# Kernel optimization log

Measured on AMD Instinct MI355X. Metric: run time of the kernel, lower is better.

The kernel has to match this reference:

```python
import jax, jax.numpy as jnp
import numpy as np

IN_F = 4096
OUT_F = 11008
GROUP = 128
NG = IN_F // GROUP  # 32 groups


def setup_inputs() -> dict:
    key = jax.random.key(0)
    k1, k2, k3, k4 = jax.random.split(key, 4)
    x = jax.random.normal(k1, (4, 2048, IN_F), dtype=jnp.float32)
    # packed 4-bit weights: 8 nibbles per int32 along the in_features axis
    qweight = jax.random.randint(k2, (IN_F // 8, OUT_F), 0, 2**31 - 1, dtype=jnp.int32)
    scales = jax.random.uniform(k3, (NG, OUT_F), dtype=jnp.float32, minval=0.001, maxval=0.02)
    # packed 4-bit zero-points: 8 nibbles per int32 along the out_features axis
    qzeros = jax.random.randint(k4, (NG, OUT_F // 8), 0, 2**31 - 1, dtype=jnp.int32)
    g_idx = (jnp.arange(IN_F) // GROUP).astype(jnp.int32)
    return {"x": x, "qweight": qweight, "scales": scales, "qzeros": qzeros, "g_idx": g_idx}


def _dequant(qweight, scales, qzeros, g_idx):
    """GPTQ v2 dequant (matches vecquant4recons_v2): W = s * (w4 - (z4 + 1))."""
    shifts = (jnp.arange(8, dtype=jnp.uint32) * 4)  # nibble shifts 0..28
    qw = jax.lax.bitcast_convert_type(qweight, jnp.uint32)  # [in/8, out]
    # unpack along in_features: [in/8, 8, out] -> [in, out]
    w4 = ((qw[:, None, :] >> shifts[None, :, None]) & jnp.uint32(0xF)).reshape(-1, qweight.shape[1])
    qz = jax.lax.bitcast_convert_type(qzeros, jnp.uint32)  # [ng, out/8]
    # unpack along out_features: [ng, out/8, 8] -> [ng, out]; GPTQ adds +1 to zero
    z4 = ((qz[:, :, None] >> shifts[None, None, :]) & jnp.uint32(0xF)).reshape(qzeros.shape[0], -1) + jnp.uint32(1)
    dt = scales.dtype
    return scales[g_idx] * (w4.astype(dt) - z4[g_idx].astype(dt))  # [in, out]


def reference(x, qweight, scales, qzeros, g_idx):
    W = _dequant(qweight, scales, qzeros, g_idx)  # [in_features, out_features]
    return jnp.matmul(x, W)  # [..., out_features]
```

## Files before the change

### kernel.cpp

```cpp
#include <hip/hip_runtime.h>
#include <hip/hip_fp16.h>
#include <stdint.h>


#define IN_F  4096
#define OUT_F 11008

typedef __attribute__((ext_vector_type(8))) _Float16 half8;
typedef __attribute__((ext_vector_type(4))) float f32x4;

__device__ __forceinline__ __half2 u2h2(uint32_t u) {
    union { uint32_t u; __half2 h; } c; c.u = u; return c.h;
}
__device__ __forceinline__ uint32_t h22u(__half2 h) {
    union { uint32_t u; __half2 h; } c; c.h = h; return c.u;
}
__device__ __forceinline__ uint32_t pkrtz(float lo, float hi) {
    union { __fp16 h[2]; uint32_t u; } c;
    *(decltype(__builtin_amdgcn_cvt_pkrtz(0.f,0.f))*)c.h =
        __builtin_amdgcn_cvt_pkrtz(lo, hi);
    return c.u;
}
__device__ __forceinline__ void async_copy16(const void* gsrc, void* ldst) {
    __builtin_amdgcn_global_load_lds(
        (const __attribute__((address_space(1))) uint32_t*)gsrc,
        (__attribute__((address_space(3))) uint32_t*)ldst,
        16, 0, 0);
}

__global__ __launch_bounds__(256) void cvt_a(
    const float* __restrict__ x, uint4* __restrict__ xh)
{
    const size_t idx = (size_t)blockIdx.x * 256 + threadIdx.x;
    const float4* p = (const float4*)(x + idx * 8);
    const float4 lo = p[0], hi = p[1];
    uint4 w;
    w.x = pkrtz(lo.x, hi.x);
    w.y = pkrtz(lo.y, hi.y);
    w.z = pkrtz(lo.z, hi.z);
    w.w = pkrtz(lo.w, hi.w);
    xh[idx] = w;
}

__global__ __launch_bounds__(512, 2) void gptq_gemm256(
    const uint4* __restrict__ xh,
    const int*   __restrict__ qweight,
    const float* __restrict__ scales,
    const int*   __restrict__ qzeros,
    float* __restrict__ out)
{
    extern __shared__ uint4 smem[];

    const int t    = threadIdx.x;
    const int lane = t & 63;
    const int wave = t >> 6;
    const int n0   = blockIdx.x * 256;
    const int m0   = blockIdx.y * 256;

    const int wm   = (wave >> 2) * 128;
    const int wn   = (wave & 3) * 64;
    const int ln15 = lane & 15;
    const int quad = lane >> 4;
    const int swz  = ln15 & 7;

    f32x4 acc[8][4];
#pragma unroll
    for (int i = 0; i < 8; ++i)
#pragma unroll
        for (int j = 0; j < 4; ++j)
            acc[i][j] = (f32x4){0.f, 0.f, 0.f, 0.f};

    const int arow_l = lane >> 3;
    const int xch    = (lane & 7) ^ arow_l;
    const char* asrc[4];
#pragma unroll
    for (int q = 0; q < 4; ++q) {
        const int m = wave * 32 + q * 8 + arow_l;
        asrc[q] = (const char*)xh + ((size_t)(m0 + m) * 512 + xch) * 16;
    }
    const int aslot = (wave * 4) * 64;

    const int b_c  = t & 255;
    const int b_r0 = t >> 8;
    const int n_th = n0 + b_c;
    const int*   qw_base = qweight + n_th;
    const float* sc_base = scales + n_th;
    const int*   qz_base = qzeros + (n_th >> 3);
    const int    z_shift = (n_th & 7) * 4;

    {
        uint32_t bw[4];
#pragma unroll
        for (int i = 0; i < 4; ++i)
            bw[i] = (uint32_t)qw_base[(size_t)(b_r0 + 2 * i) * OUT_F];
        const float    s  = sc_base[0];
        const uint32_t zw = (uint32_t)qz_base[0];
#pragma unroll
        for (int q = 0; q < 4; ++q) {
            async_copy16(asrc[q], smem + aslot + q * 64);
            asrc[q] += 128;
        }
        const __half2 s2  = u2h2(pkrtz(s, s));
        const float   bzf = (float)(((zw >> z_shift) & 0xFu) + 1025u);
        const __half2 bz2 = u2h2(pkrtz(bzf, bzf));
        uint4* Bb = smem + 4096;
#pragma unroll
        for (int i = 0; i < 4; ++i) {
            const int r = b_r0 + 2 * i;
            const uint32_t w = bw[i];
            uint32_t q0 = ( w        & 0x000F000Fu) | 0x64006400u;
            uint32_t q1 = ((w >>  4) & 0x000F000Fu) | 0x64006400u;
            uint32_t q2 = ((w >>  8) & 0x000F000Fu) | 0x64006400u;
            uint32_t q3 = ((w >> 12) & 0x000F000Fu) | 0x64006400u;
            uint4 o;
            o.x = h22u(__hmul2(__hsub2(u2h2(q0), bz2), s2));
            o.y = h22u(__hmul2(__hsub2(u2h2(q1), bz2), s2));
            o.z = h22u(__hmul2(__hsub2(u2h2(q2), bz2), s2));
            o.w = h22u(__hmul2(__hsub2(u2h2(q3), bz2), s2));
            Bb[b_c * 8 + (r ^ (b_c & 7))] = o;
        }
        __syncthreads();
    }

    for (int tile = 0; tile < 64; ++tile) {
        const int  cur = tile & 1;
        const int  nxt = cur ^ 1;
        const bool pf  = (tile < 63);

        uint32_t nbw[4]; float ns = 0.f; uint32_t nzw = 0;
        if (pf) {
            const int kq0 = (tile + 1) * 8;
#pragma unroll
            for (int i = 0; i < 4; ++i)
                nbw[i] = (uint32_t)qw_base[(size_t)(kq0 + b_r0 + 2 * i) * OUT_F];
            const int g = (tile + 1) >> 1;
            ns  = sc_base[(size_t)g * OUT_F];
            nzw = (uint32_t)qz_base[(size_t)g * (OUT_F / 8)];
            uint4* An = smem + (nxt ? 2048 : 0);
#pragma unroll
            for (int q = 0; q < 4; ++q) {
                async_copy16(asrc[q], An + aslot + q * 64);
                asrc[q] += 128;
            }
        }

        const uint4* Ac = smem + (cur ? 2048 : 0);
        const uint4* Bc = smem + 4096 + (cur ? 2048 : 0);
#pragma unroll
        for (int ks = 0; ks < 2; ++ks) {
            half8 af[8], bf[4];
#pragma unroll
            for (int i = 0; i < 8; ++i) {
                const int m  = wm + i * 16 + ln15;
                const int ch = (ks * 4 + quad) ^ swz;
                af[i] = *(const half8*)&Ac[m * 8 + ch];
            }
#pragma unroll
            for (int j = 0; j < 4; ++j) {
                const int n  = wn + j * 16 + ln15;
                const int ch = (ks * 4 + quad) ^ swz;
                bf[j] = *(const half8*)&Bc[n * 8 + ch];
            }
#pragma unroll
            for (int i = 0; i < 8; ++i)
#pragma unroll
                for (int j = 0; j < 4; ++j)
                    acc[i][j] = __builtin_amdgcn_mfma_f32_16x16x32_f16(
                        af[i], bf[j], acc[i][j], 0, 0, 0);
        }

        if (pf) {
            const __half2 s2  = u2h2(pkrtz(ns, ns));
            const float   bzf = (float)(((nzw >> z_shift) & 0xFu) + 1025u);
            const __half2 bz2 = u2h2(pkrtz(bzf, bzf));
            uint4* Bn = smem + 4096 + (nxt ? 2048 : 0);
#pragma unroll
            for (int i = 0; i < 4; ++i) {
                const int r = b_r0 + 2 * i;
                const uint32_t w = nbw[i];
                uint32_t q0 = ( w        & 0x000F000Fu) | 0x64006400u;
                uint32_t q1 = ((w >>  4) & 0x000F000Fu) | 0x64006400u;
                uint32_t q2 = ((w >>  8) & 0x000F000Fu) | 0x64006400u;
                uint32_t q3 = ((w >> 12) & 0x000F000Fu) | 0x64006400u;
                uint4 o;
                o.x = h22u(__hmul2(__hsub2(u2h2(q0), bz2), s2));
                o.y = h22u(__hmul2(__hsub2(u2h2(q1), bz2), s2));
                o.z = h22u(__hmul2(__hsub2(u2h2(q2), bz2), s2));
                o.w = h22u(__hmul2(__hsub2(u2h2(q3), bz2), s2));
                Bn[b_c * 8 + (r ^ (b_c & 7))] = o;
            }
            __syncthreads();
        }
    }

#pragma unroll
    for (int i = 0; i < 8; ++i) {
#pragma unroll
        for (int j = 0; j < 4; ++j) {
            const int col  = n0 + wn + j * 16 + ln15;
            const int row0 = m0 + wm + i * 16 + quad * 4;
            float* p = out + (size_t)row0 * OUT_F + col;
#pragma unroll
            for (int r = 0; r < 4; ++r)
                p[(size_t)r * OUT_F] = acc[i][j][r];
        }
    }
}

__global__ __launch_bounds__(256, 4) void gptq_gemm(
    const float* __restrict__ x,
    const int*   __restrict__ qweight,
    const float* __restrict__ scales,
    const int*   __restrict__ qzeros,
    float* __restrict__ out)
{
    __shared__ uint4 As[128 * 8];
    __shared__ uint4 Bs[128 * 8];

    const int t    = threadIdx.x;
    const int lane = t & 63;
    const int wave = t >> 6;
    const int n0   = blockIdx.x * 128;
    const int m0   = blockIdx.y * 128;

    const int wm   = (wave >> 1) * 64;
    const int wn   = (wave & 1) * 64;
    const int ln15 = lane & 15;
    const int quad = lane >> 4;

    f32x4 acc[4][4];
#pragma unroll
    for (int i = 0; i < 4; ++i)
#pragma unroll
        for (int j = 0; j < 4; ++j)
            acc[i][j] = (f32x4){0.f, 0.f, 0.f, 0.f};

    const int a_m0 = t >> 3;
    const int a_c8 = t & 7;
    const float* x_base = x + (size_t)(m0 + a_m0) * IN_F + a_c8 * 8;

    const int b_c  = t & 127;
    const int b_r0 = t >> 7;
    const int n_th = n0 + b_c;
    const int*   qw_base = qweight + n_th;
    const float* sc_base = scales + n_th;
    const int*   qz_base = qzeros + (n_th >> 3);
    const int    z_shift = (n_th & 7) * 4;

    for (int k0 = 0; k0 < IN_F; k0 += 64) {
        float4 av[8];
#pragma unroll
        for (int i = 0; i < 4; ++i) {
            const float* p = x_base + (size_t)(32 * i) * IN_F + k0;
            av[2 * i]     = *(const float4*)p;
            av[2 * i + 1] = *(const float4*)(p + 4);
        }
        const int kq0 = k0 >> 3;
        uint32_t bw[4];
#pragma unroll
        for (int i = 0; i < 4; ++i)
            bw[i] = (uint32_t)qw_base[(size_t)(kq0 + b_r0 + 2 * i) * OUT_F];

        const int g = k0 >> 7;
        const float    s  = sc_base[(size_t)g * OUT_F];
        const uint32_t zw = (uint32_t)qz_base[(size_t)g * (OUT_F / 8)];
        const float    bzf = (float)(((zw >> z_shift) & 0xFu) + 1025u);
        const __half2  s2  = u2h2(pkrtz(s, s));
        const __half2  bz2 = u2h2(pkrtz(bzf, bzf));

        __syncthreads();

#pragma unroll
        for (int i = 0; i < 4; ++i) {
            const int m  = a_m0 + 32 * i;
            const int ch = a_c8 ^ (m & 7);
            const float4 lo = av[2 * i], hi = av[2 * i + 1];
            uint4 w;
            w.x = pkrtz(lo.x, hi.x);
            w.y = pkrtz(lo.y, hi.y);
            w.z = pkrtz(lo.z, hi.z);
            w.w = pkrtz(lo.w, hi.w);
            As[m * 8 + ch] = w;
        }
#pragma unroll
        for (int i = 0; i < 4; ++i) {
            const int r = b_r0 + 2 * i;
            const uint32_t w = bw[i];
            uint32_t q0 = ( w        & 0x000F000Fu) | 0x64006400u;
            uint32_t q1 = ((w >>  4) & 0x000F000Fu) | 0x64006400u;
            uint32_t q2 = ((w >>  8) & 0x000F000Fu) | 0x64006400u;
            uint32_t q3 = ((w >> 12) & 0x000F000Fu) | 0x64006400u;
            uint4 o;
            o.x = h22u(__hmul2(__hsub2(u2h2(q0), bz2), s2));
            o.y = h22u(__hmul2(__hsub2(u2h2(q1), bz2), s2));
            o.z = h22u(__hmul2(__hsub2(u2h2(q2), bz2), s2));
            o.w = h22u(__hmul2(__hsub2(u2h2(q3), bz2), s2));
            const int ch = r ^ (b_c & 7);
            Bs[b_c * 8 + ch] = o;
        }
        __syncthreads();

#pragma unroll
        for (int ks = 0; ks < 2; ++ks) {
            half8 af[4], bf[4];
#pragma unroll
            for (int i = 0; i < 4; ++i) {
                const int m  = wm + i * 16 + ln15;
                const int ch = (ks * 4 + quad) ^ (m & 7);
                af[i] = *(const half8*)&As[m * 8 + ch];
            }
#pragma unroll
            for (int j = 0; j < 4; ++j) {
                const int n  = wn + j * 16 + ln15;
                const int ch = (ks * 4 + quad) ^ (n & 7);
                bf[j] = *(const half8*)&Bs[n * 8 + ch];
            }
#pragma unroll
            for (int i = 0; i < 4; ++i)
#pragma unroll
                for (int j = 0; j < 4; ++j)
                    acc[i][j] = __builtin_amdgcn_mfma_f32_16x16x32_f16(
                        af[i], bf[j], acc[i][j], 0, 0, 0);
        }
    }

#pragma unroll
    for (int i = 0; i < 4; ++i) {
#pragma unroll
        for (int j = 0; j < 4; ++j) {
            const int col  = n0 + wn + j * 16 + ln15;
            const int row0 = m0 + wm + i * 16 + quad * 4;
            float* p = out + (size_t)row0 * OUT_F + col;
#pragma unroll
            for (int r = 0; r < 4; ++r)
                p[(size_t)r * OUT_F] = acc[i][j][r];
        }
    }
}

extern "C" void kernel_launch(void* const* d_in, const int* in_sizes, int n_in,
                              void* d_out, int out_size, void* d_ws, size_t ws_size,
                              hipStream_t stream) {
    const float* x       = (const float*)d_in[0];
    const int*   qweight = (const int*)d_in[1];
    const float* scales  = (const float*)d_in[2];
    const int*   qzeros  = (const int*)d_in[3];
    float* out = (float*)d_out;

    const size_t xh_bytes = (size_t)8192 * IN_F * 2;
    if (d_ws != nullptr && ws_size >= xh_bytes) {
        static bool attr_done = false;
        if (!attr_done) {
            (void)hipFuncSetAttribute(
                reinterpret_cast<const void*>(gptq_gemm256),
                hipFuncAttributeMaxDynamicSharedMemorySize, 131072);
            attr_done = true;
        }
        uint4* xh = (uint4*)d_ws;
        cvt_a<<<(8192 * 512) / 256, 256, 0, stream>>>(x, xh);
        dim3 grid(OUT_F / 256, 8192 / 256);
        gptq_gemm256<<<grid, 512, 131072, stream>>>(xh, qweight, scales, qzeros, out);
    } else {
        dim3 grid(OUT_F / 128, 8192 / 128);
        gptq_gemm<<<grid, 256, 0, stream>>>(x, qweight, scales, qzeros, out);
    }
}
```

Baseline: 1.148 ms.

## Split tile loop into four phased MFMA blocks with barriers and priority

Restructures each K-tile into four phases, each of which reads a quarter of the A/B fragments from LDS, issues part of the async A prefetch or the B dequant, then runs 16 MFMAs under raised s_setprio between explicit barriers and waitcnts. The goal is to interleave LDS reads, global prefetch and dequant work with MFMA execution across waves, as in ping-pong scheduling. It adds several workgroup barriers per tile, which could stall waves if the phases are not balanced.

```diff
diff --git a/kernel.cpp b/kernel.cpp
--- a/kernel.cpp
+++ b/kernel.cpp
@@ -42,6 +42,32 @@
     xh[idx] = w;
 }
 
+
+#define READ_A4(DST, AC, I0, KS)                                         \
+    _Pragma("unroll") for (int i_ = 0; i_ < 4; ++i_) {                   \
+        const int m_ = wm + ((I0) + i_) * 16 + ln15;                     \
+        DST[i_] = *(const half8*)&AC[m_ * 8 + (((KS) * 4 + quad) ^ swz)];\
+    }
+#define READ_B4(DST, BC, KS)                                             \
+    _Pragma("unroll") for (int j_ = 0; j_ < 4; ++j_) {                   \
+        const int n_ = wn + j_ * 16 + ln15;                              \
+        DST[j_] = *(const half8*)&BC[n_ * 8 + (((KS) * 4 + quad) ^ swz)];\
+    }
+#define MFMA16(I0, AV, BV)                                               \
+    _Pragma("unroll") for (int i_ = 0; i_ < 4; ++i_)                     \
+    _Pragma("unroll") for (int j_ = 0; j_ < 4; ++j_)                     \
+        acc[(I0) + i_][j_] = __builtin_amdgcn_mfma_f32_16x16x32_f16(     \
+            AV[i_], BV[j_], acc[(I0) + i_][j_], 0, 0, 0);
+#define PHASE_MFMA(I0, AV, BV)                                           \
+    __builtin_amdgcn_sched_barrier(0);                                   \
+    __builtin_amdgcn_s_barrier();                                        \
+    asm volatile("s_waitcnt lgkmcnt(0)" ::: "memory");                   \
+    __builtin_amdgcn_sched_barrier(0);                                   \
+    __builtin_amdgcn_s_setprio(1);                                       \
+    MFMA16(I0, AV, BV);                                                  \
+    __builtin_amdgcn_s_setprio(0);                                       \
+    __builtin_amdgcn_sched_barrier(0);
+
 __global__ __launch_bounds__(512, 2) void gptq_gemm256(
     const uint4* __restrict__ xh,
     const int*   __restrict__ qweight,
@@ -78,7 +104,7 @@
         const int m = wave * 32 + q * 8 + arow_l;
         asrc[q] = (const char*)xh + ((size_t)(m0 + m) * 512 + xch) * 16;
     }
-    const int aslot = (wave * 4) * 64;
+    const int aslot = wave * 256;
 
     const int b_c  = t & 255;
     const int b_r0 = t >> 8;
@@ -126,8 +152,16 @@
         const int  cur = tile & 1;
         const int  nxt = cur ^ 1;
         const bool pf  = (tile < 63);
+        const uint4* Ac = smem + (cur ? 2048 : 0);
+        const uint4* Bc = smem + 4096 + (cur ? 2048 : 0);
+        uint4* An = smem + (nxt ? 2048 : 0);
+        uint4* Bn = smem + 4096 + (nxt ? 2048 : 0);
 
         uint32_t nbw[4]; float ns = 0.f; uint32_t nzw = 0;
+
+        half8 a0[4], b0[4];
+        READ_A4(a0, Ac, 0, 0);
+        READ_B4(b0, Bc, 0);
         if (pf) {
             const int kq0 = (tile + 1) * 8;
 #pragma unroll
@@ -136,44 +170,33 @@
             const int g = (tile + 1) >> 1;
             ns  = sc_base[(size_t)g * OUT_F];
             nzw = (uint32_t)qz_base[(size_t)g * (OUT_F / 8)];
-            uint4* An = smem + (nxt ? 2048 : 0);
-#pragma unroll
-            for (int q = 0; q < 4; ++q) {
-                async_copy16(asrc[q], An + aslot + q * 64);
-                asrc[q] += 128;
-            }
-        }
-
-        const uint4* Ac = smem + (cur ? 2048 : 0);
-        const uint4* Bc = smem + 4096 + (cur ? 2048 : 0);
-#pragma unroll
-        for (int ks = 0; ks < 2; ++ks) {
-            half8 af[8], bf[4];
-#pragma unroll
-            for (int i = 0; i < 8; ++i) {
-                const int m  = wm + i * 16 + ln15;
-                const int ch = (ks * 4 + quad) ^ swz;
-                af[i] = *(const half8*)&Ac[m * 8 + ch];
-            }
-#pragma unroll
-            for (int j = 0; j < 4; ++j) {
-                const int n  = wn + j * 16 + ln15;
-                const int ch = (ks * 4 + quad) ^ swz;
-                bf[j] = *(const half8*)&Bc[n * 8 + ch];
-            }
-#pragma unroll
-            for (int i = 0; i < 8; ++i)
-#pragma unroll
-                for (int j = 0; j < 4; ++j)
-                    acc[i][j] = __builtin_amdgcn_mfma_f32_16x16x32_f16(
-                        af[i], bf[j], acc[i][j], 0, 0, 0);
-        }
-
+            async_copy16(asrc[0], An + aslot);       asrc[0] += 128;
+            async_copy16(asrc[1], An + aslot + 64);  asrc[1] += 128;
+        }
+        PHASE_MFMA(0, a0, b0);
+        __builtin_amdgcn_s_barrier();
+
+        half8 a1[4];
+        READ_A4(a1, Ac, 4, 0);
+        if (pf) {
+            async_copy16(asrc[2], An + aslot + 128); asrc[2] += 128;
+            async_copy16(asrc[3], An + aslot + 192); asrc[3] += 128;
+        }
+        PHASE_MFMA(4, a1, b0);
+        __builtin_amdgcn_s_barrier();
+
+        half8 a2[4], b1[4];
+        READ_A4(a2, Ac, 0, 1);
+        READ_B4(b1, Bc, 1);
+        PHASE_MFMA(0, a2, b1);
+        __builtin_amdgcn_s_barrier();
+
+        half8 a3[4];
+        READ_A4(a3, Ac, 4, 1);
         if (pf) {
             const __half2 s2  = u2h2(pkrtz(ns, ns));
             const float   bzf = (float)(((nzw >> z_shift) & 0xFu) + 1025u);
             const __half2 bz2 = u2h2(pkrtz(bzf, bzf));
-            uint4* Bn = smem + 4096 + (nxt ? 2048 : 0);
 #pragma unroll
             for (int i = 0; i < 4; ++i) {
                 const int r = b_r0 + 2 * i;
@@ -189,8 +212,9 @@
                 o.w = h22u(__hmul2(__hsub2(u2h2(q3), bz2), s2));
                 Bn[b_c * 8 + (r ^ (b_c & 7))] = o;
             }
-            __syncthreads();
-        }
+        }
+        PHASE_MFMA(4, a3, b1);
+        __syncthreads();
     }
 
 #pragma unroll
```

Measured after the change: 1.164 ms. Within noise of the previous version (+1.3%).

## Dequantize weights directly into MFMA B-fragments in registers, drop B LDS staging

Applied to the files above, without the earlier changes.

The 256-tile kernel no longer stages dequantized weights through shared memory. Each lane now loads the packed int4 words it needs for its MFMA B operands straight from global memory and dequantizes them in registers, keeping scale and zero per column and reloading them only at group boundaries. Dynamic LDS drops from 128 KB to 64 KB, which removes the B LDS writes and reads and could allow more resident blocks. In exchange, each weight word is loaded and dequantized redundantly by every wave that shares the column, global loads become narrower and less coalesced, and register pressure rises.

```diff
diff --git a/kernel.cpp b/kernel.cpp
--- a/kernel.cpp
+++ b/kernel.cpp
@@ -5,6 +5,7 @@
 
 #define IN_F  4096
 #define OUT_F 11008
+#define QZ_W  (OUT_F / 8)
 
 typedef __attribute__((ext_vector_type(8))) _Float16 half8;
 typedef __attribute__((ext_vector_type(4))) float f32x4;
@@ -26,6 +27,18 @@
         (const __attribute__((address_space(1))) uint32_t*)gsrc,
         (__attribute__((address_space(3))) uint32_t*)ldst,
         16, 0, 0);
+}
+__device__ __forceinline__ half8 dq8(uint32_t w, __half2 bz2, __half2 s2) {
+    uint32_t q0 = ( w        & 0x000F000Fu) | 0x64006400u;
+    uint32_t q1 = ((w >>  4) & 0x000F000Fu) | 0x64006400u;
+    uint32_t q2 = ((w >>  8) & 0x000F000Fu) | 0x64006400u;
+    uint32_t q3 = ((w >> 12) & 0x000F000Fu) | 0x64006400u;
+    union { half8 h; uint32_t u[4]; } f;
+    f.u[0] = h22u(__hmul2(__hsub2(u2h2(q0), bz2), s2));
+    f.u[1] = h22u(__hmul2(__hsub2(u2h2(q1), bz2), s2));
+    f.u[2] = h22u(__hmul2(__hsub2(u2h2(q2), bz2), s2));
+    f.u[3] = h22u(__hmul2(__hsub2(u2h2(q3), bz2), s2));
+    return f.h;
 }
 
 __global__ __launch_bounds__(256) void cvt_a(
@@ -78,119 +91,112 @@
         const int m = wave * 32 + q * 8 + arow_l;
         asrc[q] = (const char*)xh + ((size_t)(m0 + m) * 512 + xch) * 16;
     }
-    const int aslot = (wave * 4) * 64;
-
-    const int b_c  = t & 255;
-    const int b_r0 = t >> 8;
-    const int n_th = n0 + b_c;
-    const int*   qw_base = qweight + n_th;
-    const float* sc_base = scales + n_th;
-    const int*   qz_base = qzeros + (n_th >> 3);
-    const int    z_shift = (n_th & 7) * 4;
-
-    {
-        uint32_t bw[4];
-#pragma unroll
-        for (int i = 0; i < 4; ++i)
-            bw[i] = (uint32_t)qw_base[(size_t)(b_r0 + 2 * i) * OUT_F];
-        const float    s  = sc_base[0];
-        const uint32_t zw = (uint32_t)qz_base[0];
-#pragma unroll
-        for (int q = 0; q < 4; ++q) {
-            async_copy16(asrc[q], smem + aslot + q * 64);
-            asrc[q] += 128;
-        }
-        const __half2 s2  = u2h2(pkrtz(s, s));
-        const float   bzf = (float)(((zw >> z_shift) & 0xFu) + 1025u);
-        const __half2 bz2 = u2h2(pkrtz(bzf, bzf));
-        uint4* Bb = smem + 4096;
-#pragma unroll
-        for (int i = 0; i < 4; ++i) {
-            const int r = b_r0 + 2 * i;
-            const uint32_t w = bw[i];
-            uint32_t q0 = ( w        & 0x000F000Fu) | 0x64006400u;
-            uint32_t q1 = ((w >>  4) & 0x000F000Fu) | 0x64006400u;
-            uint32_t q2 = ((w >>  8) & 0x000F000Fu) | 0x64006400u;
-            uint32_t q3 = ((w >> 12) & 0x000F000Fu) | 0x64006400u;
-            uint4 o;
-            o.x = h22u(__hmul2(__hsub2(u2h2(q0), bz2), s2));
-            o.y = h22u(__hmul2(__hsub2(u2h2(q1), bz2), s2));
-            o.z = h22u(__hmul2(__hsub2(u2h2(q2), bz2), s2));
-            o.w = h22u(__hmul2(__hsub2(u2h2(q3), bz2), s2));
-            Bb[b_c * 8 + (r ^ (b_c & 7))] = o;
-        }
-        __syncthreads();
-    }
+    const int aslot = wave * 256;
+
+    const int* qwp[4];
+    int sc_ix[4], qz_ix[4], zsh[4];
+#pragma unroll
+    for (int j = 0; j < 4; ++j) {
+        const int nj = n0 + wn + j * 16 + ln15;
+        qwp[j]   = qweight + (size_t)quad * OUT_F + nj;
+        sc_ix[j] = nj;
+        qz_ix[j] = nj >> 3;
+        zsh[j]   = (nj & 7) * 4;
+    }
+
+    uint32_t bw[2][4];
+#pragma unroll
+    for (int ks = 0; ks < 2; ++ks)
+#pragma unroll
+        for (int j = 0; j < 4; ++j)
+            bw[ks][j] = (uint32_t)qwp[j][(size_t)(ks * 4) * OUT_F];
+
+    __half2 s2[4], bz2[4];
+#pragma unroll
+    for (int j = 0; j < 4; ++j) {
+        const float    s  = scales[sc_ix[j]];
+        const uint32_t zw = (uint32_t)qzeros[qz_ix[j]];
+        s2[j]  = u2h2(pkrtz(s, s));
+        const float bzf = (float)(((zw >> zsh[j]) & 0xFu) + 1025u);
+        bz2[j] = u2h2(pkrtz(bzf, bzf));
+    }
+#pragma unroll
+    for (int q = 0; q < 4; ++q) {
+        async_copy16(asrc[q], smem + aslot + q * 64);
+        asrc[q] += 128;
+    }
+    __syncthreads();
 
     for (int tile = 0; tile < 64; ++tile) {
         const int  cur = tile & 1;
-        const int  nxt = cur ^ 1;
         const bool pf  = (tile < 63);
-
-        uint32_t nbw[4]; float ns = 0.f; uint32_t nzw = 0;
+        const uint4* Ac = smem + (cur ? 2048 : 0);
+        uint4* An = smem + (cur ? 0 : 2048);
+
+        uint32_t nbw[2][4];
         if (pf) {
-            const int kq0 = (tile + 1) * 8;
-#pragma unroll
-            for (int i = 0; i < 4; ++i)
-                nbw[i] = (uint32_t)qw_base[(size_t)(kq0 + b_r0 + 2 * i) * OUT_F];
-            const int g = (tile + 1) >> 1;
-            ns  = sc_base[(size_t)g * OUT_F];
-            nzw = (uint32_t)qz_base[(size_t)g * (OUT_F / 8)];
-            uint4* An = smem + (nxt ? 2048 : 0);
 #pragma unroll
             for (int q = 0; q < 4; ++q) {
                 async_copy16(asrc[q], An + aslot + q * 64);
                 asrc[q] += 128;
             }
-        }
-
-        const uint4* Ac = smem + (cur ? 2048 : 0);
-        const uint4* Bc = smem + 4096 + (cur ? 2048 : 0);
+            const size_t r0 = (size_t)(tile + 1) * 8;
+#pragma unroll
+            for (int ks = 0; ks < 2; ++ks)
+#pragma unroll
+                for (int j = 0; j < 4; ++j)
+                    nbw[ks][j] = (uint32_t)qwp[j][(r0 + ks * 4) * OUT_F];
+        }
+        const bool newg = pf && (((tile + 1) & 1) == 0);
+        float nsr[4]; uint32_t nzr[4];
+        if (newg) {
+            const size_t g1 = (size_t)(tile + 1) >> 1;
+#pragma unroll
+            for (int j = 0; j < 4; ++j) {
+                nsr[j] = scales[g1 * OUT_F + sc_ix[j]];
+                nzr[j] = (uint32_t)qzeros[g1 * QZ_W + qz_ix[j]];
+            }
+        }
+
+        half8 bf[2][4];
+#pragma unroll
+        for (int ks = 0; ks < 2; ++ks)
+#pragma unroll
+            for (int j = 0; j < 4; ++j)
+                bf[ks][j] = dq8(bw[ks][j], bz2[j], s2[j]);
+
 #pragma unroll
         for (int ks = 0; ks < 2; ++ks) {
-            half8 af[8], bf[4];
+            half8 af[8];
 #pragma unroll
             for (int i = 0; i < 8; ++i) {
-                const int m  = wm + i * 16 + ln15;
-                const int ch = (ks * 4 + quad) ^ swz;
-                af[i] = *(const half8*)&Ac[m * 8 + ch];
-            }
-#pragma unroll
-            for (int j = 0; j < 4; ++j) {
-                const int n  = wn + j * 16 + ln15;
-                const int ch = (ks * 4 + quad) ^ swz;
-                bf[j] = *(const half8*)&Bc[n * 8 + ch];
+                const int m = wm + i * 16 + ln15;
+                af[i] = *(const half8*)&Ac[m * 8 + (((ks * 4 + quad)) ^ swz)];
             }
 #pragma unroll
             for (int i = 0; i < 8; ++i)
 #pragma unroll
                 for (int j = 0; j < 4; ++j)
                     acc[i][j] = __builtin_amdgcn_mfma_f32_16x16x32_f16(
-                        af[i], bf[j], acc[i][j], 0, 0, 0);
-        }
-
+                        af[i], bf[ks][j], acc[i][j], 0, 0, 0);
+        }
+
+        if (newg) {
+#pragma unroll
+            for (int j = 0; j < 4; ++j) {
+                s2[j] = u2h2(pkrtz(nsr[j], nsr[j]));
+                const float bzf = (float)(((nzr[j] >> zsh[j]) & 0xFu) + 1025u);
+                bz2[j] = u2h2(pkrtz(bzf, bzf));
+            }
+        }
         if (pf) {
-            const __half2 s2  = u2h2(pkrtz(ns, ns));
-            const float   bzf = (float)(((nzw >> z_shift) & 0xFu) + 1025u);
-            const __half2 bz2 = u2h2(pkrtz(bzf, bzf));
-            uint4* Bn = smem + 4096 + (nxt ? 2048 : 0);
-#pragma unroll
-            for (int i = 0; i < 4; ++i) {
-                const int r = b_r0 + 2 * i;
-                const uint32_t w = nbw[i];
-                uint32_t q0 = ( w        & 0x000F000Fu) | 0x64006400u;
-                uint32_t q1 = ((w >>  4) & 0x000F000Fu) | 0x64006400u;
-                uint32_t q2 = ((w >>  8) & 0x000F000Fu) | 0x64006400u;
-                uint32_t q3 = ((w >> 12) & 0x000F000Fu) | 0x64006400u;
-                uint4 o;
-                o.x = h22u(__hmul2(__hsub2(u2h2(q0), bz2), s2));
-                o.y = h22u(__hmul2(__hsub2(u2h2(q1), bz2), s2));
-                o.z = h22u(__hmul2(__hsub2(u2h2(q2), bz2), s2));
-                o.w = h22u(__hmul2(__hsub2(u2h2(q3), bz2), s2));
-                Bn[b_c * 8 + (r ^ (b_c & 7))] = o;
-            }
-            __syncthreads();
-        }
+#pragma unroll
+            for (int ks = 0; ks < 2; ++ks)
+#pragma unroll
+                for (int j = 0; j < 4; ++j)
+                    bw[ks][j] = nbw[ks][j];
+        }
+        __syncthreads();
     }
 
 #pragma unroll
@@ -256,14 +262,14 @@
             av[2 * i + 1] = *(const float4*)(p + 4);
         }
         const int kq0 = k0 >> 3;
-        uint32_t bw[4];
+        uint32_t bwv[4];
 #pragma unroll
         for (int i = 0; i < 4; ++i)
-            bw[i] = (uint32_t)qw_base[(size_t)(kq0 + b_r0 + 2 * i) * OUT_F];
+            bwv[i] = (uint32_t)qw_base[(size_t)(kq0 + b_r0 + 2 * i) * OUT_F];
 
         const int g = k0 >> 7;
         const float    s  = sc_base[(size_t)g * OUT_F];
-        const uint32_t zw = (uint32_t)qz_base[(size_t)g * (OUT_F / 8)];
+        const uint32_t zw = (uint32_t)qz_base[(size_t)g * QZ_W];
         const float    bzf = (float)(((zw >> z_shift) & 0xFu) + 1025u);
         const __half2  s2  = u2h2(pkrtz(s, s));
         const __half2  bz2 = u2h2(pkrtz(bzf, bzf));
@@ -285,24 +291,15 @@
 #pragma unroll
         for (int i = 0; i < 4; ++i) {
             const int r = b_r0 + 2 * i;
-            const uint32_t w = bw[i];
-            uint32_t q0 = ( w        & 0x000F000Fu) | 0x64006400u;
-            uint32_t q1 = ((w >>  4) & 0x000F000Fu) | 0x64006400u;
-            uint32_t q2 = ((w >>  8) & 0x000F000Fu) | 0x64006400u;
-            uint32_t q3 = ((w >> 12) & 0x000F000Fu) | 0x64006400u;
-            uint4 o;
-            o.x = h22u(__hmul2(__hsub2(u2h2(q0), bz2), s2));
-            o.y = h22u(__hmul2(__hsub2(u2h2(q1), bz2), s2));
-            o.z = h22u(__hmul2(__hsub2(u2h2(q2), bz2), s2));
-            o.w = h22u(__hmul2(__hsub2(u2h2(q3), bz2), s2));
+            half8 o = dq8(bwv[i], bz2, s2);
             const int ch = r ^ (b_c & 7);
-            Bs[b_c * 8 + ch] = o;
+            *(half8*)&Bs[b_c * 8 + ch] = o;
         }
         __syncthreads();
 
 #pragma unroll
         for (int ks = 0; ks < 2; ++ks) {
-            half8 af[4], bf[4];
+            half8 af[4], bfv[4];
 #pragma unroll
             for (int i = 0; i < 4; ++i) {
                 const int m  = wm + i * 16 + ln15;
@@ -313,14 +310,14 @@
             for (int j = 0; j < 4; ++j) {
                 const int n  = wn + j * 16 + ln15;
                 const int ch = (ks * 4 + quad) ^ (n & 7);
-                bf[j] = *(const half8*)&Bs[n * 8 + ch];
+                bfv[j] = *(const half8*)&Bs[n * 8 + ch];
             }
 #pragma unroll
             for (int i = 0; i < 4; ++i)
 #pragma unroll
                 for (int j = 0; j < 4; ++j)
                     acc[i][j] = __builtin_amdgcn_mfma_f32_16x16x32_f16(
-                        af[i], bf[j], acc[i][j], 0, 0, 0);
+                        af[i], bfv[j], acc[i][j], 0, 0, 0);
         }
     }
 
@@ -353,13 +350,13 @@
         if (!attr_done) {
             (void)hipFuncSetAttribute(
                 reinterpret_cast<const void*>(gptq_gemm256),
-                hipFuncAttributeMaxDynamicSharedMemorySize, 131072);
+                hipFuncAttributeMaxDynamicSharedMemorySize, 65536);
             attr_done = true;
         }
         uint4* xh = (uint4*)d_ws;
         cvt_a<<<(8192 * 512) / 256, 256, 0, stream>>>(x, xh);
         dim3 grid(OUT_F / 256, 8192 / 256);
-        gptq_gemm256<<<grid, 512, 131072, stream>>>(xh, qweight, scales, qzeros, out);
+        gptq_gemm256<<<grid, 512, 65536, stream>>>(xh, qweight, scales, qzeros, out);
     } else {
         dim3 grid(OUT_F / 128, 8192 / 128);
         gptq_gemm<<<grid, 256, 0, stream>>>(x, qweight, scales, qzeros, out);
```

Result: no change. 1.130 ms (-1.6%).
